# Kernel tuning notes

Measured on AMD Instinct MI355X. Metric: run time of the kernel, lower is better.

The kernel has to match this reference:

```python
import jax, jax.numpy as jnp
import numpy as np

INPUT_SZ = 16
HPF = 32  # hidden_per_feat_sz
INTERACTIONS = [(0, 1), (2, 3), (4, 5), (6, 7)]
N_INT = len(INTERACTIONS)
INPUT_SIZE = INPUT_SZ + 2 * N_INT          # 24
HIDDEN = (INPUT_SZ + N_INT) * HPF          # 640
BATCH, SEQ = 128, 512

# static masks, faithful to the torch code (note: only even-indexed interactions
# get U_mask rows, exactly as the original loop `range(0, len(interactions), 2)`)
_Um = np.zeros((INPUT_SIZE, HIDDEN), np.float32)
for i in range(INPUT_SZ):
    _Um[i, i * HPF:(i + 1) * HPF] = 1
for i in range(0, N_INT, 2):
    _Um[i + INPUT_SZ, i * HPF:(i + 1) * HPF] = 1
    _Um[i + INPUT_SZ + 1, i * HPF:(i + 1) * HPF] = 1
U_MASK = jnp.asarray(_Um)
V_MASK = jnp.asarray(np.kron(np.eye(INPUT_SZ + N_INT, dtype=np.float32),
                             np.ones((HPF, HPF), np.float32)))
FEAT_SEQ = np.array(list(range(INPUT_SZ)) + [f for p in INTERACTIONS for f in p])


def setup_inputs() -> dict:
    key = jax.random.key(0)
    ks = jax.random.split(key, 13)
    stdv = 1.0 / np.sqrt(HIDDEN)
    u = lambda k, s: jax.random.uniform(k, s, jnp.float32, -stdv, stdv)
    inp = {"x": jax.random.normal(ks[0], (BATCH, SEQ, INPUT_SZ), jnp.float32)}
    names = ["i", "f", "c", "o"]
    for j, n in enumerate(names):
        inp[f"U_{n}"] = u(ks[1 + 3 * j], (INPUT_SIZE, HIDDEN))
        inp[f"V_{n}"] = u(ks[2 + 3 * j], (HIDDEN, HIDDEN))
        inp[f"b_{n}"] = u(ks[3 + 3 * j], (HIDDEN,))
    return inp


def reference(x, U_i, V_i, b_i, U_f, V_f, b_f, U_c, V_c, b_c, U_o, V_o, b_o):
    # gather masked-feature view of inputs once: [B, T, INPUT_SIZE]
    xg = x[:, :, FEAT_SEQ]
    # precompute masked, gate-concatenated weights (i|f|c|o)
    Ucat = jnp.concatenate([U_i * U_MASK, U_f * U_MASK,
                            U_c * U_MASK, U_o * U_MASK], axis=1)   # [in, 4H]
    Vcat = jnp.concatenate([V_i * V_MASK, V_f * V_MASK,
                            V_c * V_MASK, V_o * V_MASK], axis=1)   # [H, 4H]
    bcat = jnp.concatenate([b_i, b_f, b_c, b_o])                   # [4H]
    # input contribution for all timesteps in one GEMM: [B, T, 4H]
    xU = jnp.einsum('bti,ig->btg', xg, Ucat) + bcat

    h0 = jnp.zeros((x.shape[0], HIDDEN), x.dtype)
    c0 = jnp.zeros_like(h0)

    def step(carry, xu_t):
        h, c = carry
        gates = xu_t + h @ Vcat
        i_t, f_t, g_t, o_t = jnp.split(gates, 4, axis=-1)
        c = jax.nn.sigmoid(f_t) * c + jax.nn.sigmoid(i_t) * jnp.tanh(g_t)
        h = jax.nn.sigmoid(o_t) * jnp.tanh(c)
        return (h, c), h

    (h_t, c_t), hs = jax.lax.scan(step, (h0, c0), jnp.swapaxes(xU, 0, 1))
    hidden_seq = jnp.swapaxes(hs, 0, 1)  # [B, T, H]
    return hidden_seq, (h_t, c_t)
```

## Files before the change

kernel.cpp:

```cpp
#include <hip/hip_runtime.h>


#define TT 512
#define HN 640
#define BN 128

__device__ __forceinline__ float rl(float v, int s) {
  return __int_as_float(__builtin_amdgcn_readlane(__float_as_int(v), s));
}

__global__ __launch_bounds__(256) void lstm_kernel(
    const float* __restrict__ x,
    const float* __restrict__ Ui, const float* __restrict__ Vi, const float* __restrict__ bi,
    const float* __restrict__ Uf, const float* __restrict__ Vf, const float* __restrict__ bf,
    const float* __restrict__ Uc, const float* __restrict__ Vc, const float* __restrict__ bc,
    const float* __restrict__ Uo, const float* __restrict__ Vo, const float* __restrict__ bo,
    float* __restrict__ out) {
  const int unit = (blockIdx.x * 256 + threadIdx.x) >> 6;
  const int lane = threadIdx.x & 63;
  const int j = unit >> 7;
  const int b = unit & 127;
  const int gp = lane >> 5;
  const int n = lane & 31;
  const int col = j * 32 + n;

  const float* UG1 = gp ? Uc : Ui;
  const float* UG2 = gp ? Uo : Uf;
  const float* VG1 = gp ? Vc : Vi;
  const float* VG2 = gp ? Vo : Vf;
  const float* bG1 = gp ? bc : bi;
  const float* bG2 = gp ? bo : bf;

  float w11 = 0.f, w21 = 0.f, w12 = 0.f, w22 = 0.f;
  int f1 = 0, f2 = 0;
  if (j < 16) {
    f1 = f2 = j;
    w11 = UG1[j * HN + col];
    w12 = UG2[j * HN + col];
    if (j == 0) {
      w11 += UG1[16 * HN + col]; w12 += UG2[16 * HN + col];
      w21  = UG1[17 * HN + col]; w22  = UG2[17 * HN + col];
      f2 = 1;
    } else if (j == 2) {
      w11 += UG1[18 * HN + col]; w12 += UG2[18 * HN + col];
      w21  = UG1[19 * HN + col]; w22  = UG2[19 * HN + col];
      f2 = 3;
    }
  }
  const float bb1 = bG1[col];
  const float bb2 = bG2[col];

  float v1r[32], v2r[32];
#pragma unroll
  for (int k = 0; k < 32; ++k) {
    v1r[k] = VG1[(j * 32 + k) * HN + col];
    v2r[k] = VG2[(j * 32 + k) * HN + col];
  }

  float xa[8], xb[8];
#pragma unroll
  for (int i = 0; i < 8; ++i) {
    const int t = i * 64 + lane;
    xa[i] = x[(b * TT + t) * 16 + f1];
    xb[i] = x[(b * TT + t) * 16 + f2];
  }

  const float LOG2E = 1.44269504088896340736f;
  const float Bc1 = gp ? (-2.f * LOG2E) : -LOG2E;
  const float Ac1 = gp ? 2.f : 1.f;
  const float Cc1 = gp ? -1.f : 0.f;

  float h = 0.f, c = 0.f;
  int ob = b * TT * HN + col;
#pragma unroll
  for (int i = 0; i < 8; ++i) {
    const float xc1 = xa[i];
    const float xc2 = xb[i];
    for (int s = 0; s < 64; ++s) {
      const float x1 = rl(xc1, s);
      const float x2 = rl(xc2, s);
      float a1 = fmaf(x2, w21, fmaf(x1, w11, bb1));
      float a2 = fmaf(x2, w22, fmaf(x1, w12, bb2));
      float a1b = 0.f, a2b = 0.f;
#pragma unroll
      for (int k = 0; k < 32; k += 2) {
        const float hk0 = rl(h, k);
        const float hk1 = rl(h, k + 1);
        a1  = fmaf(hk0, v1r[k],     a1);
        a2  = fmaf(hk0, v2r[k],     a2);
        a1b = fmaf(hk1, v1r[k + 1], a1b);
        a2b = fmaf(hk1, v2r[k + 1], a2b);
      }
      a1 += a1b;
      a2 += a2b;
      const float g1 = fmaf(Ac1, __builtin_amdgcn_rcpf(1.f + __builtin_amdgcn_exp2f(Bc1 * a1)), Cc1);
      const float g2 = __builtin_amdgcn_rcpf(1.f + __builtin_amdgcn_exp2f(-LOG2E * a2));
      const float p1 = __shfl_xor(g1, 32);
      const float p2 = __shfl_xor(g2, 32);
      c = fmaf(g2, c, g1 * p1);
      const float tc = fmaf(2.f, __builtin_amdgcn_rcpf(1.f + __builtin_amdgcn_exp2f(-2.f * LOG2E * c)), -1.f);
      h = p2 * tc;
      if (lane < 32) out[ob] = h;
      ob += HN;
    }
  }
  if (lane < 32) {
    out[BN * TT * HN + b * HN + col] = h;
    out[BN * TT * HN + BN * HN + b * HN + col] = c;
  }
}

extern "C" void kernel_launch(void* const* d_in, const int* in_sizes, int n_in,
                              void* d_out, int out_size, void* d_ws, size_t ws_size,
                              hipStream_t stream) {
  (void)in_sizes; (void)n_in; (void)d_ws; (void)ws_size; (void)out_size;
  const float* x  = (const float*)d_in[0];
  const float* Ui = (const float*)d_in[1];
  const float* Vi = (const float*)d_in[2];
  const float* bi = (const float*)d_in[3];
  const float* Uf = (const float*)d_in[4];
  const float* Vf = (const float*)d_in[5];
  const float* bf = (const float*)d_in[6];
  const float* Uc = (const float*)d_in[7];
  const float* Vc = (const float*)d_in[8];
  const float* bc = (const float*)d_in[9];
  const float* Uo = (const float*)d_in[10];
  const float* Vo = (const float*)d_in[11];
  const float* bo = (const float*)d_in[12];
  float* out = (float*)d_out;

  dim3 grid(640);
  dim3 block(256);
  hipLaunchKernelGGL(lstm_kernel, grid, block, 0, stream,
                     x, Ui, Vi, bi, Uf, Vf, bf, Uc, Vc, bc, Uo, Vo, bo, out);
}
```

Baseline: 469.9 us.

## Broadcast h via LDS and use packed FMA with prescaled weights

```diff
diff --git a/kernel.cpp b/kernel.cpp
--- a/kernel.cpp
+++ b/kernel.cpp
@@ -5,19 +5,28 @@
 #define HN 640
 #define BN 128
 
+typedef float f2 __attribute__((ext_vector_type(2)));
+typedef float f4v __attribute__((ext_vector_type(4)));
+
 __device__ __forceinline__ float rl(float v, int s) {
   return __int_as_float(__builtin_amdgcn_readlane(__float_as_int(v), s));
 }
 
-__global__ __launch_bounds__(256) void lstm_kernel(
+__device__ __forceinline__ void pkfma(f2& acc, f2 w, f2 h) {
+  asm("v_pk_fma_f32 %0, %1, %2, %0" : "+v"(acc) : "v"(w), "v"(h));
+}
+
+__global__ __launch_bounds__(64) void lstm_kernel(
     const float* __restrict__ x,
     const float* __restrict__ Ui, const float* __restrict__ Vi, const float* __restrict__ bi,
     const float* __restrict__ Uf, const float* __restrict__ Vf, const float* __restrict__ bf,
     const float* __restrict__ Uc, const float* __restrict__ Vc, const float* __restrict__ bc,
     const float* __restrict__ Uo, const float* __restrict__ Vo, const float* __restrict__ bo,
     float* __restrict__ out) {
-  const int unit = (blockIdx.x * 256 + threadIdx.x) >> 6;
-  const int lane = threadIdx.x & 63;
+  __shared__ __align__(16) float hsh[64];
+
+  const int unit = blockIdx.x;
+  const int lane = threadIdx.x;
   const int j = unit >> 7;
   const int b = unit & 127;
   const int gp = lane >> 5;
@@ -31,30 +40,38 @@
   const float* bG1 = gp ? bc : bi;
   const float* bG2 = gp ? bo : bf;
 
+  const float LOG2E = 1.44269504088896340736f;
+  const float B1 = gp ? (-2.f * LOG2E) : -LOG2E;
+  const float B2 = -LOG2E;
+  const float Ac1 = gp ? 2.f : 1.f;
+  const float Cc1 = gp ? -1.f : 0.f;
+
   float w11 = 0.f, w21 = 0.f, w12 = 0.f, w22 = 0.f;
-  int f1 = 0, f2 = 0;
+  int f1 = 0, f2i = 0;
   if (j < 16) {
-    f1 = f2 = j;
+    f1 = f2i = j;
     w11 = UG1[j * HN + col];
     w12 = UG2[j * HN + col];
     if (j == 0) {
       w11 += UG1[16 * HN + col]; w12 += UG2[16 * HN + col];
       w21  = UG1[17 * HN + col]; w22  = UG2[17 * HN + col];
-      f2 = 1;
+      f2i = 1;
     } else if (j == 2) {
       w11 += UG1[18 * HN + col]; w12 += UG2[18 * HN + col];
       w21  = UG1[19 * HN + col]; w22  = UG2[19 * HN + col];
-      f2 = 3;
+      f2i = 3;
     }
   }
-  const float bb1 = bG1[col];
-  const float bb2 = bG2[col];
+  const float ws11 = B1 * w11, ws21 = B1 * w21, bs1 = B1 * bG1[col];
+  const float ws12 = B2 * w12, ws22 = B2 * w22, bs2 = B2 * bG2[col];
 
-  float v1r[32], v2r[32];
+  f2 wA[16], wB[16];
 #pragma unroll
-  for (int k = 0; k < 32; ++k) {
-    v1r[k] = VG1[(j * 32 + k) * HN + col];
-    v2r[k] = VG2[(j * 32 + k) * HN + col];
+  for (int kp = 0; kp < 16; ++kp) {
+    wA[kp].x = B1 * VG1[(j * 32 + 2 * kp) * HN + col];
+    wA[kp].y = B1 * VG1[(j * 32 + 2 * kp + 1) * HN + col];
+    wB[kp].x = B2 * VG2[(j * 32 + 2 * kp) * HN + col];
+    wB[kp].y = B2 * VG2[(j * 32 + 2 * kp + 1) * HN + col];
   }
 
   float xa[8], xb[8];
@@ -62,13 +79,8 @@
   for (int i = 0; i < 8; ++i) {
     const int t = i * 64 + lane;
     xa[i] = x[(b * TT + t) * 16 + f1];
-    xb[i] = x[(b * TT + t) * 16 + f2];
+    xb[i] = x[(b * TT + t) * 16 + f2i];
   }
-
-  const float LOG2E = 1.44269504088896340736f;
-  const float Bc1 = gp ? (-2.f * LOG2E) : -LOG2E;
-  const float Ac1 = gp ? 2.f : 1.f;
-  const float Cc1 = gp ? -1.f : 0.f;
 
   float h = 0.f, c = 0.f;
   int ob = b * TT * HN + col;
@@ -79,26 +91,38 @@
     for (int s = 0; s < 64; ++s) {
       const float x1 = rl(xc1, s);
       const float x2 = rl(xc2, s);
-      float a1 = fmaf(x2, w21, fmaf(x1, w11, bb1));
-      float a2 = fmaf(x2, w22, fmaf(x1, w12, bb2));
-      float a1b = 0.f, a2b = 0.f;
+      const float sx1 = fmaf(x2, ws21, fmaf(x1, ws11, bs1));
+      const float sx2 = fmaf(x2, ws22, fmaf(x1, ws12, bs2));
+      hsh[lane] = h;
+      __builtin_amdgcn_wave_barrier();
+      f2 hp[16];
 #pragma unroll
-      for (int k = 0; k < 32; k += 2) {
-        const float hk0 = rl(h, k);
-        const float hk1 = rl(h, k + 1);
-        a1  = fmaf(hk0, v1r[k],     a1);
-        a2  = fmaf(hk0, v2r[k],     a2);
-        a1b = fmaf(hk1, v1r[k + 1], a1b);
-        a2b = fmaf(hk1, v2r[k + 1], a2b);
+      for (int m = 0; m < 8; ++m) {
+        f4v q;
+        __builtin_memcpy(&q, &hsh[4 * m], 16);
+        hp[2 * m]     = __builtin_shufflevector(q, q, 0, 1);
+        hp[2 * m + 1] = __builtin_shufflevector(q, q, 2, 3);
       }
-      a1 += a1b;
-      a2 += a2b;
-      const float g1 = fmaf(Ac1, __builtin_amdgcn_rcpf(1.f + __builtin_amdgcn_exp2f(Bc1 * a1)), Cc1);
-      const float g2 = __builtin_amdgcn_rcpf(1.f + __builtin_amdgcn_exp2f(-LOG2E * a2));
+      __builtin_amdgcn_wave_barrier();
+      f2 aA = {sx1, 0.f}, aB = {sx2, 0.f};
+#pragma unroll
+      for (int kp = 0; kp < 16; ++kp) {
+        pkfma(aA, wA[kp], hp[kp]);
+        pkfma(aB, wB[kp], hp[kp]);
+      }
+      const float a1 = aA.x + aA.y;
+      const float a2 = aB.x + aB.y;
+      const float e1 = __builtin_amdgcn_exp2f(a1);
+      const float e2 = __builtin_amdgcn_exp2f(a2);
+      const float g1 = fmaf(Ac1, __builtin_amdgcn_rcpf(1.f + e1), Cc1);
+      const float g2 = __builtin_amdgcn_rcpf(1.f + e2);
       const float p1 = __shfl_xor(g1, 32);
       const float p2 = __shfl_xor(g2, 32);
       c = fmaf(g2, c, g1 * p1);
-      const float tc = fmaf(2.f, __builtin_amdgcn_rcpf(1.f + __builtin_amdgcn_exp2f(-2.f * LOG2E * c)), -1.f);
+      const float tc = fmaf(
+          2.f,
+          __builtin_amdgcn_rcpf(1.f + __builtin_amdgcn_exp2f(-2.f * LOG2E * c)),
+          -1.f);
       h = p2 * tc;
       if (lane < 32) out[ob] = h;
       ob += HN;
@@ -129,8 +153,8 @@
   const float* bo = (const float*)d_in[12];
   float* out = (float*)d_out;
 
-  dim3 grid(640);
-  dim3 block(256);
+  dim3 grid(2560);
+  dim3 block(64);
   hipLaunchKernelGGL(lstm_kernel, grid, block, 0, stream,
                      x, Ui, Vi, bi, Uf, Vf, bf, Uc, Vc, bc, Uo, Vo, bo, out);
 }
```

New measurement: 397.8 us. -15.3%, faster.
